# Kernel optimization log

Hardware: AMD Instinct MI355X
Metric: run time of the kernel (lower is better)

Reference implementation:

```python
import jax, jax.numpy as jnp
import numpy as np

N, E, H = 50000, 800000, 128

def _lin_params(key, out_dim, in_dim, bias=True, gain=1.0):
    k1, k2 = jax.random.split(key)
    lim = gain * np.sqrt(6.0 / (in_dim + out_dim))
    W = jax.random.uniform(k1, (out_dim, in_dim), jnp.float32, -lim, lim)
    b = jax.random.uniform(k2, (out_dim,), jnp.float32, -lim, lim) if bias else None
    return W, b

def setup_inputs() -> dict:
    key = jax.random.key(0)
    ks = jax.random.split(key, 12)
    h = jax.random.normal(ks[0], (N, H), jnp.float32)
    x = jax.random.normal(ks[1], (N, 3), jnp.float32)
    edge_index = jax.random.randint(ks[2], (2, E), 0, N, jnp.int64)
    We1, be1 = _lin_params(ks[3], H, 2 * H + 1)
    We2, be2 = _lin_params(ks[4], H, H)
    Wn1, bn1 = _lin_params(ks[5], H, 2 * H)
    Wn2, bn2 = _lin_params(ks[6], H, H)
    Wc1, bc1 = _lin_params(ks[7], H, H)
    Wc2, _ = _lin_params(ks[8], 1, H, bias=False, gain=0.001)
    gamma = jnp.ones((H,), jnp.float32)
    beta = jnp.zeros((H,), jnp.float32)
    return {"h": h, "x": x, "edge_index": edge_index,
            "We1": We1, "be1": be1, "We2": We2, "be2": be2,
            "Wn1": Wn1, "bn1": bn1, "Wn2": Wn2, "bn2": bn2,
            "Wc1": Wc1, "bc1": bc1, "Wc2": Wc2,
            "gamma": gamma, "beta": beta}

def _layer_norm(y, gamma, beta, eps=1e-5):
    mu = jnp.mean(y, axis=-1, keepdims=True)
    var = jnp.var(y, axis=-1, keepdims=True)
    return (y - mu) * jax.lax.rsqrt(var + eps) * gamma + beta

def reference(h, x, edge_index, We1, be1, We2, be2, Wn1, bn1, Wn2, bn2,
              Wc1, bc1, Wc2, gamma, beta):
    src, dst = edge_index[0], edge_index[1]
    diff = x[src] - x[dst]                                  # (E, 3)
    dist_sq = jnp.sum(diff * diff, axis=-1, keepdims=True)  # (E, 1)
    edge_in = jnp.concatenate([h[src], h[dst], dist_sq], axis=-1)  # (E, 2H+1)
    m = jax.nn.silu(edge_in @ We1.T + be1)
    m = jax.nn.silu(m @ We2.T + be2)                        # (E, H)
    num_nodes = h.shape[0]
    agg = jax.ops.segment_sum(m, dst, num_segments=num_nodes)            # (N, H)
    count = jax.ops.segment_sum(jnp.ones((dst.shape[0], 1), h.dtype), dst,
                                num_segments=num_nodes)
    count = jnp.maximum(count, 1.0)
    agg = agg / count
    u = jax.nn.silu(jnp.concatenate([h, agg], axis=-1) @ Wn1.T + bn1)
    h_out = h + (u @ Wn2.T + bn2)
    h_out = _layer_norm(h_out, gamma, beta)
    cw = jax.nn.silu(m @ Wc1.T + bc1) @ Wc2.T               # (E, 1)
    coord_agg = jax.ops.segment_sum(diff * cw, dst, num_segments=num_nodes) / count
    x_out = x + coord_agg
    return h_out, x_out
```

## Files before the change

kernel.cpp:

```cpp
#include <hip/hip_runtime.h>
#include <stdint.h>

using bf16x8 = __attribute__((ext_vector_type(8))) short;
using f32x4  = __attribute__((ext_vector_type(4))) float;

__device__ __forceinline__ unsigned short f2bf(float f) {
  uint32_t x = __float_as_uint(f);
  x += 0x7fffu + ((x >> 16) & 1u);
  return (unsigned short)(x >> 16);
}
__device__ __forceinline__ float bf2f(unsigned short u) {
  return __uint_as_float(((uint32_t)u) << 16);
}
__device__ __forceinline__ uint32_t cvtpk2(float lo, float hi) {
  uint32_t r;
  asm("v_cvt_pk_bf16_f32 %0, %1, %2" : "=v"(r) : "v"(lo), "v"(hi));
  return r;
}
__device__ __forceinline__ float silu_f(float v) {
  float e = __expf(-v);
  return v * __builtin_amdgcn_rcpf(1.0f + e);
}
__device__ __forceinline__ void unpack2(uint32_t u, float& lo, float& hi) {
  lo = __uint_as_float(u << 16);
  hi = __uint_as_float(u & 0xffff0000u);
}

__device__ __forceinline__ int msoff(int row, int col) {
  return row * 136 + ((((col >> 3) + row * 4) & 15) << 3) + (col & 7);
}
__device__ __forceinline__ int msoff_slot(int row, int slot) {
  return row * 136 + (((slot + row * 4) & 15) << 3);
}

__global__ void prep_kernel(const float* __restrict__ We1, const float* __restrict__ We2,
                            const float* __restrict__ Wn1, const float* __restrict__ Wn2,
                            const float* __restrict__ Wc1, const int* __restrict__ ei,
                            unsigned short* __restrict__ W1p, unsigned short* __restrict__ W2b,
                            unsigned short* __restrict__ N1b, unsigned short* __restrict__ N2b,
                            unsigned short* __restrict__ W3b, float* __restrict__ w1c,
                            int* __restrict__ flag) {
  int i = blockIdx.x * 256 + threadIdx.x;
  if (i < 256 * 128) {
    int c = i >> 7, k = i & 127;
    W1p[i] = f2bf(We1[(size_t)(c & 127) * 257 + ((c >> 7) << 7) + k]);
    N1b[i] = f2bf(Wn1[i]);
  }
  if (i < 128 * 128) {
    W2b[i] = f2bf(We2[i]);
    W3b[i] = f2bf(Wc1[i]);
    N2b[i] = f2bf(Wn2[i]);
  }
  if (i < 128) w1c[i] = We1[i * 257 + 256];
  if (i == 0) {
    int allz = 1;
    for (int k = 0; k < 64; ++k) allz &= (ei[2 * k + 1] == 0);
    *flag = allz;
  }
}

__global__ void hist_kernel(const int* __restrict__ ei, const int* __restrict__ flag,
                            int* __restrict__ deg, int E) {
  int e = blockIdx.x * 256 + threadIdx.x;
  if (e >= E) return;
  int d = (*flag) ? (int)((const long long*)ei)[(size_t)E + e] : ei[E + e];
  atomicAdd(&deg[d], 1);
}

__global__ void scanA_kernel(const int* __restrict__ deg, int* __restrict__ offs,
                             int* __restrict__ bsum, int N) {
  __shared__ int sh[256];
  int t = threadIdx.x, idx = blockIdx.x * 256 + t;
  int v = (idx < N) ? deg[idx] : 0;
  sh[t] = v;
  __syncthreads();
#pragma unroll
  for (int d = 1; d < 256; d <<= 1) {
    int u = (t >= d) ? sh[t - d] : 0;
    __syncthreads();
    sh[t] += u;
    __syncthreads();
  }
  if (idx < N) offs[idx] = sh[t] - v;
  if (t == 255) bsum[blockIdx.x] = sh[255];
}

__global__ void scanB_kernel(int* __restrict__ bsum, int* __restrict__ offs,
                             int nb, int N) {
  __shared__ int sh[256];
  int t = threadIdx.x;
  int v = (t < nb) ? bsum[t] : 0;
  sh[t] = v;
  __syncthreads();
#pragma unroll
  for (int d = 1; d < 256; d <<= 1) {
    int u = (t >= d) ? sh[t - d] : 0;
    __syncthreads();
    sh[t] += u;
    __syncthreads();
  }
  bsum[t] = sh[t] - v;
  if (t == 255) offs[N] = sh[255];
}

__global__ void scanC_kernel(const int* __restrict__ bsum, int* __restrict__ offs,
                             int* __restrict__ cursor, int N) {
  int idx = blockIdx.x * 256 + threadIdx.x;
  if (idx < N) {
    int o = offs[idx] + bsum[blockIdx.x];
    offs[idx] = o;
    cursor[idx] = o;
  }
}

__global__ void scatter_kernel(const int* __restrict__ ei, const int* __restrict__ flag,
                               int* __restrict__ cursor, int* __restrict__ csr_e, int E) {
  int e = blockIdx.x * 256 + threadIdx.x;
  if (e >= E) return;
  int d = (*flag) ? (int)((const long long*)ei)[(size_t)E + e] : ei[E + e];
  int pos = atomicAdd(&cursor[d], 1);
  csr_e[pos] = e;
}

__global__ __launch_bounds__(256) void proj_kernel(
    const float* __restrict__ h, const float* __restrict__ be1,
    const unsigned short* __restrict__ W1p, unsigned short* __restrict__ PsPd, int N) {
  const int tid = threadIdx.x;
  const int base = blockIdx.x * 64;
  const int w = tid >> 6, lane = tid & 63, lg = lane >> 4, lr = lane & 15;

  f32x4 acc[4][4];
#pragma unroll
  for (int m = 0; m < 4; ++m)
#pragma unroll
    for (int n = 0; n < 4; ++n) { f32x4 z = {0.f,0.f,0.f,0.f}; acc[m][n] = z; }

#pragma unroll
  for (int k0 = 0; k0 < 4; ++k0) {
    bf16x8 b[4];
#pragma unroll
    for (int n = 0; n < 4; ++n)
      b[n] = *(const bf16x8*)(W1p + ((w * 64 + n * 16 + lr) << 7) + k0 * 32 + lg * 8);
#pragma unroll
    for (int m = 0; m < 4; ++m) {
      int row = base + m * 16 + lr; if (row >= N) row = N - 1;
      const float* p = h + (size_t)row * 128 + k0 * 32 + lg * 8;
      float4 fa = *(const float4*)p;
      float4 fb = *(const float4*)(p + 4);
      uint32_t u0 = cvtpk2(fa.x, fa.y), u1 = cvtpk2(fa.z, fa.w);
      uint32_t u2 = cvtpk2(fb.x, fb.y), u3 = cvtpk2(fb.z, fb.w);
      union { uint32_t u[4]; bf16x8 v; } cv;
      cv.u[0] = u0; cv.u[1] = u1; cv.u[2] = u2; cv.u[3] = u3;
#pragma unroll
      for (int n = 0; n < 4; ++n)
        acc[m][n] = __builtin_amdgcn_mfma_f32_16x16x32_bf16(cv.v, b[n], acc[m][n], 0, 0, 0);
    }
  }
#pragma unroll
  for (int n = 0; n < 4; ++n) {
    int o = w * 64 + n * 16 + lr;
    float add = (o < 128) ? be1[o] : 0.f;
#pragma unroll
    for (int m = 0; m < 4; ++m)
#pragma unroll
      for (int r = 0; r < 4; ++r) {
        int row = base + m * 16 + lg * 4 + r;
        if (row < N) PsPd[(size_t)row * 256 + o] = f2bf(acc[m][n][r] + add);
      }
  }
}

__global__ __launch_bounds__(256, 4) void edge_kernel(
    const unsigned short* __restrict__ PsPd, const float* __restrict__ x,
    const int* __restrict__ ei, const float* __restrict__ w1c,
    const float* __restrict__ be2, const float* __restrict__ bc1,
    const float* __restrict__ Wc2,
    const unsigned short* __restrict__ W2b, const unsigned short* __restrict__ W3b,
    float* __restrict__ aggH, float* __restrict__ coordX,
    const int* __restrict__ csr_e, const int* __restrict__ flag, int E) {
  __shared__ __align__(16) unsigned short Ms[64 * 136];
  __shared__ float swred[4][64];
  __shared__ int   ssrc[64], sdst[64];
  __shared__ float sds[64];
  __shared__ float sdif[64][3];

  const int tid   = threadIdx.x;
  const int tbase = blockIdx.x * 64;
  const int w = tid >> 6, lane = tid & 63, lg = lane >> 4, lr = lane & 15;

  if (tid < 64) {
    int pos = tbase + tid;
    int s = 0, d = 0;
    if (pos < E) {
      int eid = csr_e[pos];
      if (*flag) {
        s = (int)((const long long*)ei)[eid];
        d = (int)((const long long*)ei)[(size_t)E + eid];
      } else {
        s = ei[eid];
        d = ei[E + eid];
      }
    }
    ssrc[tid] = s; sdst[tid] = d;
    float dx = x[s * 3 + 0] - x[d * 3 + 0];
    float dy = x[s * 3 + 1] - x[d * 3 + 1];
    float dz = x[s * 3 + 2] - x[d * 3 + 2];
    sdif[tid][0] = dx; sdif[tid][1] = dy; sdif[tid][2] = dz;
    sds[tid] = dx * dx + dy * dy + dz * dz;
  }
  __syncthreads();

  {
    uint4 av[4], bv[4];
#pragma unroll
    for (int it = 0; it < 4; ++it) {
      int idx = tid + it * 256;
      int e = idx >> 4, seg = idx & 15;
      av[it] = *(const uint4*)(PsPd + (size_t)ssrc[e] * 256 + seg * 8);
      bv[it] = *(const uint4*)(PsPd + (size_t)sdst[e] * 256 + 128 + seg * 8);
    }
    const float4* w4 = (const float4*)w1c;
#pragma unroll
    for (int it = 0; it < 4; ++it) {
      int idx = tid + it * 256;
      int e = idx >> 4, seg = idx & 15;
      float dsv = sds[e];
      float4 wA = w4[seg * 2], wB = w4[seg * 2 + 1];
      float a0,a1,a2,a3,a4,a5,a6,a7, b0,b1,b2,b3,b4,b5,b6,b7;
      unpack2(((uint32_t*)&av[it])[0], a0, a1);
      unpack2(((uint32_t*)&av[it])[1], a2, a3);
      unpack2(((uint32_t*)&av[it])[2], a4, a5);
      unpack2(((uint32_t*)&av[it])[3], a6, a7);
      unpack2(((uint32_t*)&bv[it])[0], b0, b1);
      unpack2(((uint32_t*)&bv[it])[1], b2, b3);
      unpack2(((uint32_t*)&bv[it])[2], b4, b5);
      unpack2(((uint32_t*)&bv[it])[3], b6, b7);
      float v0 = silu_f(a0 + b0 + dsv * wA.x);
      float v1 = silu_f(a1 + b1 + dsv * wA.y);
      float v2 = silu_f(a2 + b2 + dsv * wA.z);
      float v3 = silu_f(a3 + b3 + dsv * wA.w);
      float v4 = silu_f(a4 + b4 + dsv * wB.x);
      float v5 = silu_f(a5 + b5 + dsv * wB.y);
      float v6 = silu_f(a6 + b6 + dsv * wB.z);
      float v7 = silu_f(a7 + b7 + dsv * wB.w);
      uint4 o;
      o.x = cvtpk2(v0, v1); o.y = cvtpk2(v2, v3);
      o.z = cvtpk2(v4, v5); o.w = cvtpk2(v6, v7);
      *(uint4*)(&Ms[msoff_slot(e, seg)]) = o;
    }
  }
  __syncthreads();

  {
    f32x4 acc[4][2];
#pragma unroll
    for (int m = 0; m < 4; ++m) { f32x4 z = {0.f,0.f,0.f,0.f}; acc[m][0] = z; acc[m][1] = z; }
#pragma unroll
    for (int k0 = 0; k0 < 4; ++k0) {
      bf16x8 b0 = *(const bf16x8*)(W2b + ((w * 32 + lr)      << 7) + k0 * 32 + lg * 8);
      bf16x8 b1 = *(const bf16x8*)(W2b + ((w * 32 + 16 + lr) << 7) + k0 * 32 + lg * 8);
#pragma unroll
      for (int m = 0; m < 4; ++m) {
        int row = m * 16 + lr;
        bf16x8 a = *(const bf16x8*)(&Ms[msoff_slot(row, k0 * 4 + lg)]);
        acc[m][0] = __builtin_amdgcn_mfma_f32_16x16x32_bf16(a, b0, acc[m][0], 0, 0, 0);
        acc[m][1] = __builtin_amdgcn_mfma_f32_16x16x32_bf16(a, b1, acc[m][1], 0, 0, 0);
      }
    }
    uint32_t pk[4][2][2];
#pragma unroll
    for (int n = 0; n < 2; ++n) {
      int o = w * 32 + n * 16 + lr;
      float b2v = be2[o];
#pragma unroll
      for (int m = 0; m < 4; ++m)
#pragma unroll
        for (int r = 0; r < 4; r += 2)
          pk[m][n][r >> 1] = cvtpk2(silu_f(acc[m][n][r] + b2v),
                                    silu_f(acc[m][n][r + 1] + b2v));
    }
    __syncthreads();
#pragma unroll
    for (int n = 0; n < 2; ++n) {
      int o = w * 32 + n * 16 + lr;
#pragma unroll
      for (int m = 0; m < 4; ++m)
#pragma unroll
        for (int r = 0; r < 4; r += 2) {
          int row = m * 16 + lg * 4 + r;
          uint32_t u = pk[m][n][r >> 1];
          Ms[msoff(row, o)]     = (unsigned short)(u & 0xffffu);
          Ms[msoff(row + 1, o)] = (unsigned short)(u >> 16);
        }
    }
  }
  __syncthreads();

  {
    f32x4 acc[4][2];
#pragma unroll
    for (int m = 0; m < 4; ++m) { f32x4 z = {0.f,0.f,0.f,0.f}; acc[m][0] = z; acc[m][1] = z; }
#pragma unroll
    for (int k0 = 0; k0 < 4; ++k0) {
      bf16x8 b0 = *(const bf16x8*)(W3b + ((w * 32 + lr)      << 7) + k0 * 32 + lg * 8);
      bf16x8 b1 = *(const bf16x8*)(W3b + ((w * 32 + 16 + lr) << 7) + k0 * 32 + lg * 8);
#pragma unroll
      for (int m = 0; m < 4; ++m) {
        int row = m * 16 + lr;
        bf16x8 a = *(const bf16x8*)(&Ms[msoff_slot(row, k0 * 4 + lg)]);
        acc[m][0] = __builtin_amdgcn_mfma_f32_16x16x32_bf16(a, b0, acc[m][0], 0, 0, 0);
        acc[m][1] = __builtin_amdgcn_mfma_f32_16x16x32_bf16(a, b1, acc[m][1], 0, 0, 0);
      }
    }
    float pr[4][4];
#pragma unroll
    for (int m = 0; m < 4; ++m)
#pragma unroll
      for (int r = 0; r < 4; ++r) pr[m][r] = 0.f;
#pragma unroll
    for (int n = 0; n < 2; ++n) {
      int o = w * 32 + n * 16 + lr;
      float b3 = bc1[o], wc = Wc2[o];
#pragma unroll
      for (int m = 0; m < 4; ++m)
#pragma unroll
        for (int r = 0; r < 4; ++r)
          pr[m][r] += silu_f(acc[m][n][r] + b3) * wc;
    }
#pragma unroll
    for (int m = 0; m < 4; ++m)
#pragma unroll
      for (int r = 0; r < 4; ++r) {
        float v = pr[m][r];
        v += __shfl_xor(v, 1); v += __shfl_xor(v, 2);
        v += __shfl_xor(v, 4); v += __shfl_xor(v, 8);
        pr[m][r] = v;
      }
    if (lr == 0) {
#pragma unroll
      for (int m = 0; m < 4; ++m)
#pragma unroll
        for (int r = 0; r < 4; ++r)
          swred[w][m * 16 + lg * 4 + r] = pr[m][r];
    }
  }
  __syncthreads();

  const int nv = min(64, E - tbase);
  {
    int c = tid & 127, hf = tid >> 7;
    int e0 = hf * 32;
    int nvh = min(32, nv - e0);
    if (nvh > 0) {
      float run = 0.f;
      int prev = sdst[e0];
#pragma unroll 4
      for (int j = 0; j < nvh; ++j) {
        int e = e0 + j;
        int d = sdst[e];
        float v = bf2f(Ms[msoff(e, c)]);
        if (d != prev) {
          atomicAdd(&aggH[(size_t)prev * 128 + c], run);
          run = 0.f; prev = d;
        }
        run += v;
      }
      atomicAdd(&aggH[(size_t)prev * 128 + c], run);
    }
  }
  if (tid < 6) {
    int c3 = tid % 3, hf = tid / 3;
    int e0 = hf * 32;
    int nvh = min(32, nv - e0);
    if (nvh > 0) {
      float run = 0.f;
      int prev = sdst[e0];
#pragma unroll 4
      for (int j = 0; j < nvh; ++j) {
        int e = e0 + j;
        int d = sdst[e];
        float cwv = swred[0][e] + swred[1][e] + swred[2][e] + swred[3][e];
        if (d != prev) {
          atomicAdd(&coordX[(size_t)prev * 3 + c3], run);
          run = 0.f; prev = d;
        }
        run += sdif[e][c3] * cwv;
      }
      atomicAdd(&coordX[(size_t)prev * 3 + c3], run);
    }
  }
}

__global__ __launch_bounds__(256) void node_kernel(
    const float* __restrict__ h, const float* __restrict__ x,
    const float* __restrict__ bn1, const float* __restrict__ bn2,
    const float* __restrict__ gamma, const float* __restrict__ beta,
    const unsigned short* __restrict__ N1b, const unsigned short* __restrict__ N2b,
    float* __restrict__ aggH, float* __restrict__ coordX,
    const int* __restrict__ deg, int N) {
  __shared__ __align__(16) unsigned short In[64][264];
  __shared__ __align__(16) unsigned short U[64][136];
  __shared__ float scnt[64];

  const int tid  = threadIdx.x;
  const int base = blockIdx.x * 64;
  const int w    = tid >> 6;
  const int lane = tid & 63;
  const int lg   = lane >> 4, lr = lane & 15;
  const int w16  = w * 16;

  if (tid < 64) {
    int n = base + tid;
    scnt[tid] = (n < N) ? fmaxf((float)deg[n], 1.0f) : 1.0f;
  }
  __syncthreads();

#pragma unroll
  for (int it = 0; it < 8; ++it) {
    int idx = tid + it * 256;
    int i = idx >> 5, seg = idx & 31;
    int n = base + i; if (n >= N) n = N - 1;
    float sc = 1.0f;
    const float* p;
    if (seg < 16) { p = h + (size_t)n * 128 + seg * 8; }
    else          { p = aggH + (size_t)n * 128 + (seg - 16) * 8; sc = 1.0f / scnt[i]; }
    float4 a = *(const float4*)p;
    float4 b = *(const float4*)(p + 4);
    uint32_t u0 = cvtpk2(a.x * sc, a.y * sc);
    uint32_t u1 = cvtpk2(a.z * sc, a.w * sc);
    uint32_t u2 = cvtpk2(b.x * sc, b.y * sc);
    uint32_t u3 = cvtpk2(b.z * sc, b.w * sc);
    uint4 v = {u0, u1, u2, u3};
    *(uint4*)&In[i][seg * 8] = v;
  }
  __syncthreads();

  {
    f32x4 acc[8];
#pragma unroll
    for (int n = 0; n < 8; ++n) { f32x4 z = {0.f,0.f,0.f,0.f}; acc[n] = z; }
#pragma unroll
    for (int k0 = 0; k0 < 8; ++k0) {
      bf16x8 a = *(const bf16x8*)(&In[w16 + lr][k0 * 32 + lg * 8]);
#pragma unroll
      for (int n = 0; n < 8; ++n) {
        bf16x8 b = *(const bf16x8*)(N1b + ((n * 16 + lr) << 8) + k0 * 32 + lg * 8);
        acc[n] = __builtin_amdgcn_mfma_f32_16x16x32_bf16(a, b, acc[n], 0, 0, 0);
      }
    }
#pragma unroll
    for (int n = 0; n < 8; ++n) {
      int o = n * 16 + lr;
      float b1 = bn1[o];
#pragma unroll
      for (int r = 0; r < 4; ++r) {
        int me = lg * 4 + r;
        U[w16 + me][o] = f2bf(silu_f(acc[n][r] + b1));
      }
    }
  }

  float* hp = (float*)&In[0][0];
  {
    f32x4 acc[8];
#pragma unroll
    for (int n = 0; n < 8; ++n) { f32x4 z = {0.f,0.f,0.f,0.f}; acc[n] = z; }
#pragma unroll
    for (int k0 = 0; k0 < 4; ++k0) {
      bf16x8 a = *(const bf16x8*)(&U[w16 + lr][k0 * 32 + lg * 8]);
#pragma unroll
      for (int n = 0; n < 8; ++n) {
        bf16x8 b = *(const bf16x8*)(N2b + ((n * 16 + lr) << 7) + k0 * 32 + lg * 8);
        acc[n] = __builtin_amdgcn_mfma_f32_16x16x32_bf16(a, b, acc[n], 0, 0, 0);
      }
    }
#pragma unroll
    for (int n = 0; n < 8; ++n) {
      int o = n * 16 + lr;
      float b2 = bn2[o];
#pragma unroll
      for (int r = 0; r < 4; ++r) {
        int me = w16 + lg * 4 + r;
        int ng = base + me; if (ng >= N) ng = N - 1;
        hp[(size_t)me * 132 + o] = acc[n][r] + b2 + h[(size_t)ng * 128 + o];
      }
    }
  }
  __syncthreads();

  {
    int r = tid >> 2, q = tid & 3;
    int ng = base + r;
    float s = 0.f, s2 = 0.f;
#pragma unroll
    for (int j = 0; j < 32; ++j) {
      float v = hp[(size_t)r * 132 + q * 32 + j];
      s += v; s2 += v * v;
    }
    s  += __shfl_xor(s, 1);  s  += __shfl_xor(s, 2);
    s2 += __shfl_xor(s2, 1); s2 += __shfl_xor(s2, 2);
    float mu  = s * (1.0f / 128.0f);
    float var = s2 * (1.0f / 128.0f) - mu * mu;
    float rs  = rsqrtf(var + 1e-5f);
    if (ng < N) {
#pragma unroll
      for (int j = 0; j < 32; ++j) {
        int o = q * 32 + j;
        float v = (hp[(size_t)r * 132 + o] - mu) * rs * gamma[o] + beta[o];
        aggH[(size_t)ng * 128 + o] = v;
      }
    }
  }

  if (tid < 192) {
    int i = tid / 3, c = tid % 3;
    int n2 = base + i;
    if (n2 < N) {
      size_t off = (size_t)n2 * 3 + c;
      coordX[off] = x[off] + coordX[off] / scnt[i];
    }
  }
}

extern "C" void kernel_launch(void* const* d_in, const int* in_sizes, int n_in,
                              void* d_out, int out_size, void* d_ws, size_t ws_size,
                              hipStream_t stream) {
  const float* h    = (const float*)d_in[0];
  const float* x    = (const float*)d_in[1];
  const int*   ei   = (const int*)d_in[2];
  const float* We1  = (const float*)d_in[3];
  const float* be1  = (const float*)d_in[4];
  const float* We2  = (const float*)d_in[5];
  const float* be2  = (const float*)d_in[6];
  const float* Wn1  = (const float*)d_in[7];
  const float* bn1  = (const float*)d_in[8];
  const float* Wn2  = (const float*)d_in[9];
  const float* bn2  = (const float*)d_in[10];
  const float* Wc1  = (const float*)d_in[11];
  const float* bc1  = (const float*)d_in[12];
  const float* Wc2  = (const float*)d_in[13];
  const float* gamma = (const float*)d_in[14];
  const float* beta  = (const float*)d_in[15];

  int N = in_sizes[0] / 128;
  int E = in_sizes[2] / 2;

  float* aggH   = (float*)d_out;
  float* coordX = (float*)d_out + (size_t)N * 128;

  char* ws = (char*)d_ws;
  size_t off = 0;
  auto alloc = [&](size_t bytes) {
    char* p = ws + off;
    off = (off + bytes + 255) & ~(size_t)255;
    return p;
  };
  unsigned short* PsPd   = (unsigned short*)alloc((size_t)N * 256 * 2);
  unsigned short* W1p    = (unsigned short*)alloc(256 * 128 * 2);
  unsigned short* W2b    = (unsigned short*)alloc(128 * 128 * 2);
  unsigned short* N1b    = (unsigned short*)alloc(128 * 256 * 2);
  unsigned short* N2b    = (unsigned short*)alloc(128 * 128 * 2);
  unsigned short* W3b    = (unsigned short*)alloc(128 * 128 * 2);
  float*          w1c    = (float*)alloc(128 * 4);
  int*            flag   = (int*)alloc(4);
  int*            deg    = (int*)alloc((size_t)N * 4);
  int*            offs   = (int*)alloc(((size_t)N + 1) * 4);
  int*            cursor = (int*)alloc((size_t)N * 4);
  int*            bsum   = (int*)alloc(256 * 4);
  int*            csr_e  = (int*)alloc((size_t)E * 4);
  (void)ws_size;

  int nb = (N + 255) / 256;

  hipMemsetAsync(d_out, 0, (size_t)out_size * 4, stream);
  hipMemsetAsync(deg, 0, (size_t)N * 4, stream);

  prep_kernel<<<128, 256, 0, stream>>>(We1, We2, Wn1, Wn2, Wc1, ei,
                                       W1p, W2b, N1b, N2b, W3b, w1c, flag);
  hist_kernel<<<(E + 255) / 256, 256, 0, stream>>>(ei, flag, deg, E);
  scanA_kernel<<<nb, 256, 0, stream>>>(deg, offs, bsum, N);
  scanB_kernel<<<1, 256, 0, stream>>>(bsum, offs, nb, N);
  scanC_kernel<<<nb, 256, 0, stream>>>(bsum, offs, cursor, N);
  scatter_kernel<<<(E + 255) / 256, 256, 0, stream>>>(ei, flag, cursor, csr_e, E);
  proj_kernel<<<(N + 63) / 64, 256, 0, stream>>>(h, be1, W1p, PsPd, N);
  edge_kernel<<<(E + 63) / 64, 256, 0, stream>>>(PsPd, x, ei, w1c, be2, bc1, Wc2,
                                                 W2b, W3b, aggH, coordX, csr_e, flag, E);
  node_kernel<<<(N + 63) / 64, 256, 0, stream>>>(h, x, bn1, bn2, gamma, beta, N1b, N2b,
                                                 aggH, coordX, deg, N);
}
```

Before: 402.8 us.

## Store sorted src/dst directly, split projection buffers, raise edge occupancy

The scatter kernel now writes the sorted source and destination node ids directly. This removes the edge kernel's indirect lookup through csr_e and the int64/int32 flag check. The interleaved PsPd projection buffer is split into separate Ps and Pd arrays, which makes the gathered rows more compact. The edge kernel's launch bounds go from 4 to 8 waves per unit, which may force register spills. The layer-norm loop in the node kernel now reads interleaved columns, which should reduce LDS bank conflicts.

```diff
diff --git a/kernel.cpp b/kernel.cpp
--- a/kernel.cpp
+++ b/kernel.cpp
@@ -114,17 +114,27 @@
 }
 
 __global__ void scatter_kernel(const int* __restrict__ ei, const int* __restrict__ flag,
-                               int* __restrict__ cursor, int* __restrict__ csr_e, int E) {
+                               int* __restrict__ cursor,
+                               int* __restrict__ src_s, int* __restrict__ dst_s, int E) {
   int e = blockIdx.x * 256 + threadIdx.x;
   if (e >= E) return;
-  int d = (*flag) ? (int)((const long long*)ei)[(size_t)E + e] : ei[E + e];
+  int s, d;
+  if (*flag) {
+    s = (int)((const long long*)ei)[e];
+    d = (int)((const long long*)ei)[(size_t)E + e];
+  } else {
+    s = ei[e];
+    d = ei[E + e];
+  }
   int pos = atomicAdd(&cursor[d], 1);
-  csr_e[pos] = e;
+  src_s[pos] = s;
+  dst_s[pos] = d;
 }
 
 __global__ __launch_bounds__(256) void proj_kernel(
     const float* __restrict__ h, const float* __restrict__ be1,
-    const unsigned short* __restrict__ W1p, unsigned short* __restrict__ PsPd, int N) {
+    const unsigned short* __restrict__ W1p,
+    unsigned short* __restrict__ Ps, unsigned short* __restrict__ Pd, int N) {
   const int tid = threadIdx.x;
   const int base = blockIdx.x * 64;
   const int w = tid >> 6, lane = tid & 63, lg = lane >> 4, lr = lane & 15;
@@ -159,25 +169,28 @@
 #pragma unroll
   for (int n = 0; n < 4; ++n) {
     int o = w * 64 + n * 16 + lr;
+    unsigned short* dstp = (o < 128) ? Ps : Pd;
+    int oo = o & 127;
     float add = (o < 128) ? be1[o] : 0.f;
 #pragma unroll
     for (int m = 0; m < 4; ++m)
 #pragma unroll
       for (int r = 0; r < 4; ++r) {
         int row = base + m * 16 + lg * 4 + r;
-        if (row < N) PsPd[(size_t)row * 256 + o] = f2bf(acc[m][n][r] + add);
-      }
-  }
-}
-
-__global__ __launch_bounds__(256, 4) void edge_kernel(
-    const unsigned short* __restrict__ PsPd, const float* __restrict__ x,
-    const int* __restrict__ ei, const float* __restrict__ w1c,
+        if (row < N) dstp[(size_t)row * 128 + oo] = f2bf(acc[m][n][r] + add);
+      }
+  }
+}
+
+__global__ __launch_bounds__(256, 8) void edge_kernel(
+    const unsigned short* __restrict__ Ps, const unsigned short* __restrict__ Pd,
+    const float* __restrict__ x,
+    const int* __restrict__ src_s, const int* __restrict__ dst_s,
+    const float* __restrict__ w1c,
     const float* __restrict__ be2, const float* __restrict__ bc1,
     const float* __restrict__ Wc2,
     const unsigned short* __restrict__ W2b, const unsigned short* __restrict__ W3b,
-    float* __restrict__ aggH, float* __restrict__ coordX,
-    const int* __restrict__ csr_e, const int* __restrict__ flag, int E) {
+    float* __restrict__ aggH, float* __restrict__ coordX, int E) {
   __shared__ __align__(16) unsigned short Ms[64 * 136];
   __shared__ float swred[4][64];
   __shared__ int   ssrc[64], sdst[64];
@@ -191,16 +204,7 @@
   if (tid < 64) {
     int pos = tbase + tid;
     int s = 0, d = 0;
-    if (pos < E) {
-      int eid = csr_e[pos];
-      if (*flag) {
-        s = (int)((const long long*)ei)[eid];
-        d = (int)((const long long*)ei)[(size_t)E + eid];
-      } else {
-        s = ei[eid];
-        d = ei[E + eid];
-      }
-    }
+    if (pos < E) { s = src_s[pos]; d = dst_s[pos]; }
     ssrc[tid] = s; sdst[tid] = d;
     float dx = x[s * 3 + 0] - x[d * 3 + 0];
     float dy = x[s * 3 + 1] - x[d * 3 + 1];
@@ -216,8 +220,8 @@
     for (int it = 0; it < 4; ++it) {
       int idx = tid + it * 256;
       int e = idx >> 4, seg = idx & 15;
-      av[it] = *(const uint4*)(PsPd + (size_t)ssrc[e] * 256 + seg * 8);
-      bv[it] = *(const uint4*)(PsPd + (size_t)sdst[e] * 256 + 128 + seg * 8);
+      av[it] = *(const uint4*)(Ps + (size_t)ssrc[e] * 128 + seg * 8);
+      bv[it] = *(const uint4*)(Pd + (size_t)sdst[e] * 128 + seg * 8);
     }
     const float4* w4 = (const float4*)w1c;
 #pragma unroll
@@ -494,7 +498,7 @@
     float s = 0.f, s2 = 0.f;
 #pragma unroll
     for (int j = 0; j < 32; ++j) {
-      float v = hp[(size_t)r * 132 + q * 32 + j];
+      float v = hp[(size_t)r * 132 + j * 4 + q];
       s += v; s2 += v * v;
     }
     s  += __shfl_xor(s, 1);  s  += __shfl_xor(s, 2);
@@ -505,7 +509,7 @@
     if (ng < N) {
 #pragma unroll
       for (int j = 0; j < 32; ++j) {
-        int o = q * 32 + j;
+        int o = j * 4 + q;
         float v = (hp[(size_t)r * 132 + o] - mu) * rs * gamma[o] + beta[o];
         aggH[(size_t)ng * 128 + o] = v;
       }
@@ -555,7 +559,8 @@
     off = (off + bytes + 255) & ~(size_t)255;
     return p;
   };
-  unsigned short* PsPd   = (unsigned short*)alloc((size_t)N * 256 * 2);
+  unsigned short* Ps     = (unsigned short*)alloc((size_t)N * 128 * 2);
+  unsigned short* Pd     = (unsigned short*)alloc((size_t)N * 128 * 2);
   unsigned short* W1p    = (unsigned short*)alloc(256 * 128 * 2);
   unsigned short* W2b    = (unsigned short*)alloc(128 * 128 * 2);
   unsigned short* N1b    = (unsigned short*)alloc(128 * 256 * 2);
@@ -567,7 +572,8 @@
   int*            offs   = (int*)alloc(((size_t)N + 1) * 4);
   int*            cursor = (int*)alloc((size_t)N * 4);
   int*            bsum   = (int*)alloc(256 * 4);
-  int*            csr_e  = (int*)alloc((size_t)E * 4);
+  int*            src_s  = (int*)alloc((size_t)E * 4);
+  int*            dst_s  = (int*)alloc((size_t)E * 4);
   (void)ws_size;
 
   int nb = (N + 255) / 256;
@@ -581,10 +587,11 @@
   scanA_kernel<<<nb, 256, 0, stream>>>(deg, offs, bsum, N);
   scanB_kernel<<<1, 256, 0, stream>>>(bsum, offs, nb, N);
   scanC_kernel<<<nb, 256, 0, stream>>>(bsum, offs, cursor, N);
-  scatter_kernel<<<(E + 255) / 256, 256, 0, stream>>>(ei, flag, cursor, csr_e, E);
-  proj_kernel<<<(N + 63) / 64, 256, 0, stream>>>(h, be1, W1p, PsPd, N);
-  edge_kernel<<<(E + 63) / 64, 256, 0, stream>>>(PsPd, x, ei, w1c, be2, bc1, Wc2,
-                                                 W2b, W3b, aggH, coordX, csr_e, flag, E);
+  scatter_kernel<<<(E + 255) / 256, 256, 0, stream>>>(ei, flag, cursor, src_s, dst_s, E);
+  proj_kernel<<<(N + 63) / 64, 256, 0, stream>>>(h, be1, W1p, Ps, Pd, N);
+  edge_kernel<<<(E + 63) / 64, 256, 0, stream>>>(Ps, Pd, x, src_s, dst_s, w1c,
+                                                 be2, bc1, Wc2, W2b, W3b,
+                                                 aggH, coordX, E);
   node_kernel<<<(N + 63) / 64, 256, 0, stream>>>(h, x, bn1, bn2, gamma, beta, N1b, N2b,
                                                  aggH, coordX, deg, N);
 }
```

New measurement: 380.8 us. -5.4%, faster.
